# Performance work log

Measured on AMD Instinct MI355X. Metric: run time of the kernel, lower is better.

The kernel has to match this reference:

```python
import jax, jax.numpy as jnp
import numpy as np
from jax import lax

CHUNK = 128
EPS = 1e-6


def rmsnorm(x, w, eps=EPS):
    var = jnp.mean(jnp.square(x.astype(jnp.float32)), axis=-1, keepdims=True)
    return (x * lax.rsqrt(var + eps)).astype(x.dtype) * w


def linear_attn(q, k, v, slopes):
    """Decay-based (lightning/RetNet-style) causal linear attention.
    q,k,v: [B,H,S,D]; slopes: [H,1,1] positive per-head decay rates.
    out[i] = sum_{j<=i} exp(-s*(i-j)) * (q_i . k_j) * v_j, via chunked scan.
    """
    B, H, S, D = q.shape
    C = CHUNK
    nC = S // C
    s = slopes.reshape(1, H, 1, 1).astype(jnp.float32)  # [1,H,1,1]
    t = jnp.arange(C, dtype=jnp.float32)
    q_dec = jnp.exp(-s * t[None, None, :, None])            # [1,H,C,1] decay for inter-chunk query
    k_dec = jnp.exp(-s * (C - t)[None, None, :, None])      # [1,H,C,1] decay applied to keys entering state
    chunk_dec = jnp.exp(-s * C)                              # [1,H,1,1] whole-chunk state decay
    rel = t[:, None] - t[None, :]                            # [C,C]
    intra_dec = jnp.where(rel >= 0, jnp.exp(-s * rel), 0.0)  # [1,H,C,C] causal intra-chunk decay

    # [nC,B,H,C,D]
    qc = q.reshape(B, H, nC, C, D).transpose(2, 0, 1, 3, 4)
    kc = k.reshape(B, H, nC, C, D).transpose(2, 0, 1, 3, 4)
    vc = v.reshape(B, H, nC, C, D).transpose(2, 0, 1, 3, 4)

    def step(kv, inp):
        qi, ki, vi = inp  # each [B,H,C,D]; kv: [B,H,D,D]
        inter = jnp.einsum('bhcd,bhde->bhce', qi * q_dec, kv)
        scores = jnp.einsum('bhcd,bhed->bhce', qi, ki) * intra_dec  # [B,H,C,C]
        intra = jnp.einsum('bhce,bhed->bhcd', scores, vi)
        kv_new = chunk_dec * kv + jnp.einsum('bhcd,bhce->bhde', ki * k_dec, vi)
        return kv_new, inter + intra

    kv0 = jnp.zeros((B, H, D, D), dtype=jnp.float32)
    _, out = lax.scan(step, kv0, (qc, kc, vc))  # out: [nC,B,H,C,D]
    return out.transpose(1, 2, 0, 3, 4).reshape(B, H, S, D)


def setup_inputs() -> dict:
    key = jax.random.key(0)
    ks = jax.random.split(key, 8)
    B, S, E, H, D = 2, 2048, 2048, 16, 128
    init = 0.02
    hidden_states = jax.random.normal(ks[0], (B, S, E), dtype=jnp.float32)
    attention_mask = jnp.ones((B, S), dtype=jnp.float32)
    # standard ALiBi-like per-head slopes in (0,1]
    slope_rate = (2.0 ** (-8.0 * (jnp.arange(H, dtype=jnp.float32) + 1.0) / H)).reshape(H, 1, 1)
    Wq = jax.random.normal(ks[1], (E, H * D), dtype=jnp.float32) * init
    Wk = jax.random.normal(ks[2], (E, H * D), dtype=jnp.float32) * init
    Wv = jax.random.normal(ks[3], (E, H * D), dtype=jnp.float32) * init
    Wg = jax.random.normal(ks[4], (E, H * D), dtype=jnp.float32) * init
    Wo = jax.random.normal(ks[5], (H * D, E), dtype=jnp.float32) * init
    norm_w = jnp.ones((H * D,), dtype=jnp.float32)
    return {"hidden_states": hidden_states, "attention_mask": attention_mask,
            "slope_rate": slope_rate, "Wq": Wq, "Wk": Wk, "Wv": Wv,
            "Wg": Wg, "Wo": Wo, "norm_w": norm_w}


def reference(hidden_states, attention_mask, slope_rate, Wq, Wk, Wv, Wg, Wo, norm_w):
    B, S, E = hidden_states.shape
    H = slope_rate.shape[0]
    D = Wq.shape[1] // H
    q = (hidden_states @ Wq).reshape(B, S, H, D).transpose(0, 2, 1, 3)
    k = (hidden_states @ Wk).reshape(B, S, H, D).transpose(0, 2, 1, 3)
    v = (hidden_states @ Wv).reshape(B, S, H, D).transpose(0, 2, 1, 3)
    v = v * attention_mask[:, None, :, None]
    out = linear_attn(q, k, v, slope_rate)                      # [B,H,S,D]
    out = out.transpose(0, 2, 1, 3).reshape(B, S, H * D)        # b h n d -> b n (h d)
    out = rmsnorm(out, norm_w)
    out = jax.nn.sigmoid(hidden_states @ Wg) * out
    return out @ Wo
```

## Files before the change

### kernel.cpp

```cpp
#include <hip/hip_runtime.h>
#include <cstdint>
#include <cstddef>

typedef unsigned short u16;
typedef unsigned int   u32;

#define SEQ    2048
#define EDIM   2048
#define HEADS  16
#define DHEAD  128
#define CCH    128
#define NCH    16
#define TOKENS 4096

typedef __attribute__((ext_vector_type(8))) short short8;
typedef __attribute__((ext_vector_type(4))) float floatx4;

__device__ __forceinline__ float b2f(u16 b) {
    u32 u = ((u32)b) << 16; float f; __builtin_memcpy(&f, &u, 4); return f;
}
__device__ __forceinline__ u16 f2b(float f) {
    u32 u; __builtin_memcpy(&u, &f, 4);
    u32 r = (u + 0x7fffu + ((u >> 16) & 1u)) >> 16;
    return (u16)r;
}
__device__ __forceinline__ void unpack8(uint4 u, float* f) {
    f[0] = b2f((u16)(u.x & 0xffff)); f[1] = b2f((u16)(u.x >> 16));
    f[2] = b2f((u16)(u.y & 0xffff)); f[3] = b2f((u16)(u.y >> 16));
    f[4] = b2f((u16)(u.z & 0xffff)); f[5] = b2f((u16)(u.z >> 16));
    f[6] = b2f((u16)(u.w & 0xffff)); f[7] = b2f((u16)(u.w >> 16));
}
__device__ __forceinline__ uint4 pack8(const float* f) {
    uint4 u;
    u.x = (u32)f2b(f[0]) | ((u32)f2b(f[1]) << 16);
    u.y = (u32)f2b(f[2]) | ((u32)f2b(f[3]) << 16);
    u.z = (u32)f2b(f[4]) | ((u32)f2b(f[5]) << 16);
    u.w = (u32)f2b(f[6]) | ((u32)f2b(f[7]) << 16);
    return u;
}

__device__ __forceinline__ void gld_lds16(const u16* g, u16* l) {
    __builtin_amdgcn_global_load_lds((const __attribute__((address_space(1))) void*)g,
                                     (__attribute__((address_space(3))) void*)l, 16, 0, 0);
}

__global__ __launch_bounds__(256) void k_f32_to_bf16(const float* __restrict__ in,
                                                     u16* __restrict__ out) {
    int i = blockIdx.x * 256 + threadIdx.x;
    float4 v = ((const float4*)in)[i];
    uint2 o;
    o.x = (u32)f2b(v.x) | ((u32)f2b(v.y) << 16);
    o.y = (u32)f2b(v.z) | ((u32)f2b(v.w) << 16);
    ((uint2*)out)[i] = o;
}

__global__ void k_transW(const float* __restrict__ W0, const float* __restrict__ W1,
                         const float* __restrict__ W2, const float* __restrict__ W3,
                         const float* __restrict__ W4, u16* __restrict__ out) {
    const float* W;
    int z = blockIdx.z;
    switch (z) {
        case 0: W = W0; break; case 1: W = W1; break; case 2: W = W2; break;
        case 3: W = W3; break; default: W = W4; break;
    }
    __shared__ float tile[32][33];
    int n = blockIdx.x * 32 + threadIdx.x;
    int k = blockIdx.y * 32 + threadIdx.y;
    tile[threadIdx.y][threadIdx.x] = W[(size_t)k * EDIM + n];
    __syncthreads();
    int on = blockIdx.x * 32 + threadIdx.y;
    int ok = blockIdx.y * 32 + threadIdx.x;
    out[(size_t)z * EDIM * EDIM + (size_t)on * EDIM + ok] = f2b(tile[threadIdx.x][threadIdx.y]);
}

__global__ __launch_bounds__(256) void k_gemm(const u16* __restrict__ A,
                                              const u16* __restrict__ Bt,
                                              void* __restrict__ C,
                                              int K, int N,
                                              long long zstrB, long long zstrC,
                                              int out_bf16, int mode,
                                              u16* __restrict__ KdT,
                                              u16* __restrict__ VT,
                                              const float* __restrict__ slopes,
                                              const float* __restrict__ mask) {
    __shared__ u16 As[128 * 64];
    __shared__ u16 Bs[128 * 64];
    int z = blockIdx.z;
    const u16* Bz = Bt + (size_t)z * (size_t)zstrB;
    int m0 = blockIdx.y * 128, n0 = blockIdx.x * 128;
    int tid = threadIdx.x;
    int w = tid >> 6, lane = tid & 63;
    int wr = w >> 1, wc = w & 1;
    int lrow = lane & 15, khalf = lane >> 4;

    floatx4 acc[4][4];
#pragma unroll
    for (int i = 0; i < 4; i++)
#pragma unroll
        for (int j = 0; j < 4; j++) acc[i][j] = (floatx4){0.f, 0.f, 0.f, 0.f};

    const u16* aptr[4];
    const u16* bptr[4];
#pragma unroll
    for (int i = 0; i < 4; i++) {
        int c = tid + i * 256;
        int row = c >> 3, slot = c & 7;
        int g = slot ^ (row & 7);
        aptr[i] = A  + (size_t)(m0 + row) * K + g * 8;
        bptr[i] = Bz + (size_t)(n0 + row) * K + g * 8;
    }
    int aoff[2][4], boff[2][4];
#pragma unroll
    for (int kk = 0; kk < 2; kk++)
#pragma unroll
        for (int i = 0; i < 4; i++) {
            int ra = wr * 64 + i * 16 + lrow;
            int rb = wc * 64 + i * 16 + lrow;
            int gg = kk * 4 + khalf;
            aoff[kk][i] = ra * 64 + ((gg ^ (ra & 7)) * 8);
            boff[kk][i] = rb * 64 + ((gg ^ (rb & 7)) * 8);
        }

    for (int k0 = 0; k0 < K; k0 += 64) {
#pragma unroll
        for (int i = 0; i < 4; i++) {
            gld_lds16(aptr[i] + k0, &As[(tid + i * 256) * 8]);
            gld_lds16(bptr[i] + k0, &Bs[(tid + i * 256) * 8]);
        }
        __syncthreads();
#pragma unroll
        for (int kk = 0; kk < 2; kk++) {
            short8 af[4], bfr[4];
#pragma unroll
            for (int i = 0; i < 4; i++) af[i]  = *(const short8*)&As[aoff[kk][i]];
#pragma unroll
            for (int j = 0; j < 4; j++) bfr[j] = *(const short8*)&Bs[boff[kk][j]];
#pragma unroll
            for (int i = 0; i < 4; i++)
#pragma unroll
                for (int j = 0; j < 4; j++)
                    acc[i][j] = __builtin_amdgcn_mfma_f32_16x16x32_bf16(af[i], bfr[j], acc[i][j], 0, 0, 0);
        }
        __syncthreads();
    }

    int writeVT  = (mode == 1 && z == 2);
    int writeKdT = (mode == 1 && z == 1);

    if (!writeVT) {
        size_t cz = (size_t)z * (size_t)zstrC;
#pragma unroll
        for (int i = 0; i < 4; i++)
#pragma unroll
            for (int j = 0; j < 4; j++) {
                int mrow = m0 + wr * 64 + i * 16 + khalf * 4;
                int ncol = n0 + wc * 64 + j * 16 + lrow;
#pragma unroll
                for (int r = 0; r < 4; r++) {
                    float val = acc[i][j][r];
                    if (out_bf16)
                        ((u16*)C)[cz + (size_t)(mrow + r) * N + ncol] = f2b(val);
                    else
                        ((float*)C)[cz + (size_t)(mrow + r) * N + ncol] = val;
                }
            }
    }
    if (writeVT || writeKdT) {
        int b = blockIdx.y >> 4, cc = blockIdx.y & 15, h = blockIdx.x;
        size_t tile = ((size_t)b * 256 + (size_t)h * 16 + (size_t)cc) * 16384;
        float s = slopes[h];
        u16* dst = (writeVT ? VT : KdT) + tile;
#pragma unroll
        for (int i = 0; i < 4; i++)
#pragma unroll
            for (int j = 0; j < 4; j++) {
                int t0 = wr * 64 + i * 16 + khalf * 4;
                int d  = wc * 64 + j * 16 + lrow;
                u16 pk[4];
#pragma unroll
                for (int r = 0; r < 4; r++) {
                    int t = t0 + r;
                    float sc = writeVT ? mask[(size_t)b * SEQ + cc * CCH + t]
                                       : __expf(-s * (float)(CCH - t));
                    pk[r] = f2b(acc[i][j][r] * sc);
                }
                *(uint2*)&dst[(size_t)d * 128 + t0] = *(const uint2*)pk;
            }
    }
}

__global__ __launch_bounds__(256) void k_kvc(const u16* __restrict__ VT,
                                             const u16* __restrict__ KdT,
                                             u16* __restrict__ kvT) {
    int bid = blockIdx.x, tid = threadIdx.x;
    int w = tid >> 6, lane = tid & 63;
    int wr = w >> 1, wc = w & 1;
    int lrow = lane & 15, khalf = lane >> 4;
    const u16* va = VT  + (size_t)bid * 16384;
    const u16* kb = KdT + (size_t)bid * 16384;
    floatx4 acc[4][4];
#pragma unroll
    for (int i = 0; i < 4; i++)
#pragma unroll
        for (int j = 0; j < 4; j++) acc[i][j] = (floatx4){0.f, 0.f, 0.f, 0.f};
#pragma unroll
    for (int kk = 0; kk < 4; kk++) {
        short8 a[4], bf[4];
#pragma unroll
        for (int i = 0; i < 4; i++)
            a[i] = *(const short8*)(va + (size_t)(wr * 64 + i * 16 + lrow) * 128 + kk * 32 + khalf * 8);
#pragma unroll
        for (int j = 0; j < 4; j++)
            bf[j] = *(const short8*)(kb + (size_t)(wc * 64 + j * 16 + lrow) * 128 + kk * 32 + khalf * 8);
#pragma unroll
        for (int i = 0; i < 4; i++)
#pragma unroll
            for (int j = 0; j < 4; j++)
                acc[i][j] = __builtin_amdgcn_mfma_f32_16x16x32_bf16(a[i], bf[j], acc[i][j], 0, 0, 0);
    }
    u16* o = kvT + (size_t)bid * 16384;
#pragma unroll
    for (int i = 0; i < 4; i++)
#pragma unroll
        for (int j = 0; j < 4; j++)
#pragma unroll
            for (int r = 0; r < 4; r++)
                o[(size_t)(wr * 64 + i * 16 + khalf * 4 + r) * 128 + wc * 64 + j * 16 + lrow] =
                    f2b(acc[i][j][r]);
}

__global__ __launch_bounds__(256) void k_scan(u16* __restrict__ kvbuf,
                                              const float* __restrict__ slopes) {
    int gid = blockIdx.x * 256 + threadIdx.x;
    int idx = gid & 16383;
    int bh = gid >> 14;
    int h = bh & 15;
    float cd = __expf(-slopes[h] * (float)CCH);
    u16* p = kvbuf + (size_t)bh * NCH * 16384 + idx;
    float st = 0.f;
    for (int c = 0; c < NCH; c++) {
        float tmp = b2f(p[(size_t)c * 16384]);
        p[(size_t)c * 16384] = f2b(st);
        st = cd * st + tmp;
    }
}

__global__ __launch_bounds__(256) void k_attn_out(const u16* __restrict__ q,
                                                  const u16* __restrict__ k,
                                                  const u16* __restrict__ VT,
                                                  const u16* __restrict__ kvT,
                                                  const float* __restrict__ slopes,
                                                  u16* __restrict__ attn) {
    __shared__ u16 KS[128 * 136];
    int bid = blockIdx.x;
    int c = bid & 15, h = (bid >> 4) & 15, b = bid >> 8;
    float s = slopes[h];
    int tid = threadIdx.x;
    int w = tid >> 6, lane = tid & 63;
    int wr = w >> 1, wc = w & 1;
    int lrow = lane & 15, khalf = lane >> 4;
    size_t tokbase = (size_t)(b * SEQ + c * CCH);

    {
        const u16* kg = k + tokbase * EDIM + h * DHEAD;
#pragma unroll
        for (int i = 0; i < 8; i++) {
            int cidx = tid + i * 256;
            int t = cidx >> 4, part = (cidx & 15) * 8;
            *(uint4*)&KS[t * 136 + part] = *(const uint4*)(kg + (size_t)t * EDIM + part);
        }
    }
    short8 qa[4][4];
    {
        const u16* qgbase = q + tokbase * EDIM + h * DHEAD;
#pragma unroll
        for (int i = 0; i < 4; i++) {
            const u16* qrow = qgbase + (size_t)(wr * 64 + i * 16 + lrow) * EDIM;
#pragma unroll
            for (int kk = 0; kk < 4; kk++)
                qa[i][kk] = *(const short8*)(qrow + kk * 32 + khalf * 8);
        }
    }
    __syncthreads();

    floatx4 acc[4][4];
#pragma unroll
    for (int i = 0; i < 4; i++)
#pragma unroll
        for (int j = 0; j < 4; j++) acc[i][j] = (floatx4){0.f, 0.f, 0.f, 0.f};
#pragma unroll
    for (int kk = 0; kk < 4; kk++) {
        short8 bf[4];
#pragma unroll
        for (int j = 0; j < 4; j++)
            bf[j] = *(const short8*)&KS[(wc * 64 + j * 16 + lrow) * 136 + kk * 32 + khalf * 8];
#pragma unroll
        for (int i = 0; i < 4; i++)
#pragma unroll
            for (int j = 0; j < 4; j++)
                acc[i][j] = __builtin_amdgcn_mfma_f32_16x16x32_bf16(qa[i][kk], bf[j], acc[i][j], 0, 0, 0);
    }
    __syncthreads();

#pragma unroll
    for (int i = 0; i < 4; i++)
#pragma unroll
        for (int j = 0; j < 4; j++) {
            int tbase = wr * 64 + i * 16 + khalf * 4;
            int u = wc * 64 + j * 16 + lrow;
#pragma unroll
            for (int r = 0; r < 4; r++) {
                int t = tbase + r;
                float val = (t >= u) ? acc[i][j][r] * __expf(-s * (float)(t - u)) : 0.f;
                KS[t * 136 + u] = f2b(val);
            }
        }
    __syncthreads();

#pragma unroll
    for (int i = 0; i < 4; i++)
#pragma unroll
        for (int j = 0; j < 4; j++) acc[i][j] = (floatx4){0.f, 0.f, 0.f, 0.f};
    const u16* st = kvT + (size_t)bid * 16384;
#pragma unroll
    for (int kk = 0; kk < 4; kk++) {
        short8 bf[4];
#pragma unroll
        for (int j = 0; j < 4; j++)
            bf[j] = *(const short8*)(st + (size_t)(wc * 64 + j * 16 + lrow) * 128 + kk * 32 + khalf * 8);
#pragma unroll
        for (int i = 0; i < 4; i++)
#pragma unroll
            for (int j = 0; j < 4; j++)
                acc[i][j] = __builtin_amdgcn_mfma_f32_16x16x32_bf16(qa[i][kk], bf[j], acc[i][j], 0, 0, 0);
    }
#pragma unroll
    for (int i = 0; i < 4; i++)
#pragma unroll
        for (int r = 0; r < 4; r++) {
            float qd = __expf(-s * (float)(wr * 64 + i * 16 + khalf * 4 + r));
#pragma unroll
            for (int j = 0; j < 4; j++) acc[i][j][r] *= qd;
        }
    const u16* vt = VT + (size_t)bid * 16384;
#pragma unroll
    for (int kk = 0; kk < 4; kk++) {
        short8 sa[4], bf[4];
#pragma unroll
        for (int i = 0; i < 4; i++)
            sa[i] = *(const short8*)&KS[(wr * 64 + i * 16 + lrow) * 136 + kk * 32 + khalf * 8];
#pragma unroll
        for (int j = 0; j < 4; j++)
            bf[j] = *(const short8*)(vt + (size_t)(wc * 64 + j * 16 + lrow) * 128 + kk * 32 + khalf * 8);
#pragma unroll
        for (int i = 0; i < 4; i++)
#pragma unroll
            for (int j = 0; j < 4; j++)
                acc[i][j] = __builtin_amdgcn_mfma_f32_16x16x32_bf16(sa[i], bf[j], acc[i][j], 0, 0, 0);
    }

    u16* og = attn + tokbase * EDIM + h * DHEAD;
#pragma unroll
    for (int i = 0; i < 4; i++)
#pragma unroll
        for (int j = 0; j < 4; j++)
#pragma unroll
            for (int r = 0; r < 4; r++)
                og[(size_t)(wr * 64 + i * 16 + khalf * 4 + r) * EDIM + wc * 64 + j * 16 + lrow] =
                    f2b(acc[i][j][r]);
}

__global__ __launch_bounds__(256) void k_rms_gate(const u16* __restrict__ attn,
                                                  const u16* __restrict__ gpre,
                                                  const float* __restrict__ nw,
                                                  u16* __restrict__ out) {
    int n = blockIdx.x, tid = threadIdx.x;
    float a[8];
    unpack8(((const uint4*)(attn + (size_t)n * EDIM))[tid], a);
    float ss = 0.f;
#pragma unroll
    for (int j = 0; j < 8; j++) ss += a[j] * a[j];
#pragma unroll
    for (int o = 32; o > 0; o >>= 1) ss += __shfl_down(ss, o, 64);
    __shared__ float red[5];
    int w = tid >> 6, lane = tid & 63;
    if (lane == 0) red[w] = ss;
    __syncthreads();
    if (tid == 0) red[4] = rsqrtf((red[0] + red[1] + red[2] + red[3]) / 2048.f + 1e-6f);
    __syncthreads();
    float rs = red[4];
    float g[8];
    unpack8(((const uint4*)(gpre + (size_t)n * EDIM))[tid], g);
    const float4* np4 = (const float4*)(nw + tid * 8);
    float4 w0 = np4[0], w1 = np4[1];
    float wv[8] = {w0.x, w0.y, w0.z, w0.w, w1.x, w1.y, w1.z, w1.w};
    float o8[8];
#pragma unroll
    for (int j = 0; j < 8; j++) {
        float sg = 1.f / (1.f + __expf(-g[j]));
        o8[j] = sg * (a[j] * rs * wv[j]);
    }
    ((uint4*)(out + (size_t)n * EDIM))[tid] = pack8(o8);
}

extern "C" void kernel_launch(void* const* d_in, const int* in_sizes, int n_in,
                              void* d_out, int out_size, void* d_ws, size_t ws_size,
                              hipStream_t stream) {
    const float* hs     = (const float*)d_in[0];
    const float* mask   = (const float*)d_in[1];
    const float* slopes = (const float*)d_in[2];
    const float* Wq     = (const float*)d_in[3];
    const float* Wk     = (const float*)d_in[4];
    const float* Wv     = (const float*)d_in[5];
    const float* Wg     = (const float*)d_in[6];
    const float* Wo     = (const float*)d_in[7];
    const float* nw     = (const float*)d_in[8];
    float* out = (float*)d_out;

    char* ws = (char*)d_ws;
    u16* hsb   = (u16*)ws;
    u16* Wt    = (u16*)(ws + 16777216LL);
    u16* qkvg  = (u16*)(ws + 58720256LL);
    u16* kvbuf = (u16*)(ws + 125829120LL);
    u16* attn  = (u16*)(ws + 142606336LL);
    u16* qb  = qkvg;
    u16* kb  = qkvg + 8388608LL;
    u16* VT  = qkvg + 16777216LL;
    u16* gb  = qkvg + 25165824LL;
    u16* KdT = attn;

    k_f32_to_bf16<<<8192, 256, 0, stream>>>(hs, hsb);
    k_transW<<<dim3(64, 64, 5), dim3(32, 32, 1), 0, stream>>>(Wq, Wk, Wv, Wg, Wo, Wt);
    k_gemm<<<dim3(16, 32, 4), 256, 0, stream>>>(hsb, Wt, qkvg, EDIM, EDIM,
                                                (long long)EDIM * EDIM,
                                                (long long)TOKENS * EDIM, 1,
                                                1, KdT, VT, slopes, mask);
    k_kvc<<<512, 256, 0, stream>>>(VT, KdT, kvbuf);
    k_scan<<<2048, 256, 0, stream>>>(kvbuf, slopes);
    k_attn_out<<<512, 256, 0, stream>>>(qb, kb, VT, kvbuf, slopes, attn);
    k_rms_gate<<<TOKENS, 256, 0, stream>>>(attn, gb, nw, hsb);
    k_gemm<<<dim3(16, 32, 1), 256, 0, stream>>>(hsb, Wt + 4LL * 4194304LL, out, EDIM, EDIM,
                                                0LL, 0LL, 0,
                                                0, (u16*)nullptr, (u16*)nullptr, slopes, mask);
}
```

Measured before the change: 458.1 us.

## Double-buffer GEMM LDS tiles with async prefetch and manual waitcnt

Replaces the single-buffered 64-wide K tile in the bf16 GEMM with two 32-wide LDS buffers. The loads for the tile two steps ahead are issued before compute, and raw barriers with vmcnt waits keep one load group in flight, so global-to-LDS transfer overlaps MFMA work. The LDS swizzle is adapted to the 32-wide rows, and launch bounds request 4 blocks per CU to raise occupancy. This trades fewer MFMAs per barrier and the fragility of hand-coded waitcnt values for the overlap.

```diff
diff --git a/kernel.cpp b/kernel.cpp
--- a/kernel.cpp
+++ b/kernel.cpp
@@ -43,6 +43,8 @@
     __builtin_amdgcn_global_load_lds((const __attribute__((address_space(1))) void*)g,
                                      (__attribute__((address_space(3))) void*)l, 16, 0, 0);
 }
+#define CFENCE() __asm__ volatile("" ::: "memory")
+#define RAW_BARRIER() do { CFENCE(); __builtin_amdgcn_s_barrier(); CFENCE(); } while (0)
 
 __global__ __launch_bounds__(256) void k_f32_to_bf16(const float* __restrict__ in,
                                                      u16* __restrict__ out) {
@@ -73,18 +75,18 @@
     out[(size_t)z * EDIM * EDIM + (size_t)on * EDIM + ok] = f2b(tile[threadIdx.x][threadIdx.y]);
 }
 
-__global__ __launch_bounds__(256) void k_gemm(const u16* __restrict__ A,
-                                              const u16* __restrict__ Bt,
-                                              void* __restrict__ C,
-                                              int K, int N,
-                                              long long zstrB, long long zstrC,
-                                              int out_bf16, int mode,
-                                              u16* __restrict__ KdT,
-                                              u16* __restrict__ VT,
-                                              const float* __restrict__ slopes,
-                                              const float* __restrict__ mask) {
-    __shared__ u16 As[128 * 64];
-    __shared__ u16 Bs[128 * 64];
+__global__ __launch_bounds__(256, 4) void k_gemm(const u16* __restrict__ A,
+                                                 const u16* __restrict__ Bt,
+                                                 void* __restrict__ C,
+                                                 int K, int N,
+                                                 long long zstrB, long long zstrC,
+                                                 int out_bf16, int mode,
+                                                 u16* __restrict__ KdT,
+                                                 u16* __restrict__ VT,
+                                                 const float* __restrict__ slopes,
+                                                 const float* __restrict__ mask) {
+    __shared__ u16 As[2][128 * 32];
+    __shared__ u16 Bs[2][128 * 32];
     int z = blockIdx.z;
     const u16* Bz = Bt + (size_t)z * (size_t)zstrB;
     int m0 = blockIdx.y * 128, n0 = blockIdx.x * 128;
@@ -99,49 +101,60 @@
 #pragma unroll
         for (int j = 0; j < 4; j++) acc[i][j] = (floatx4){0.f, 0.f, 0.f, 0.f};
 
-    const u16* aptr[4];
-    const u16* bptr[4];
-#pragma unroll
-    for (int i = 0; i < 4; i++) {
+    const u16* aptr[2];
+    const u16* bptr[2];
+    int loff[2];
+#pragma unroll
+    for (int i = 0; i < 2; i++) {
         int c = tid + i * 256;
-        int row = c >> 3, slot = c & 7;
-        int g = slot ^ (row & 7);
+        int row = c >> 2, slot = c & 3;
+        int g = slot ^ ((row >> 1) & 3);
         aptr[i] = A  + (size_t)(m0 + row) * K + g * 8;
         bptr[i] = Bz + (size_t)(n0 + row) * K + g * 8;
-    }
-    int aoff[2][4], boff[2][4];
-#pragma unroll
-    for (int kk = 0; kk < 2; kk++)
-#pragma unroll
-        for (int i = 0; i < 4; i++) {
-            int ra = wr * 64 + i * 16 + lrow;
-            int rb = wc * 64 + i * 16 + lrow;
-            int gg = kk * 4 + khalf;
-            aoff[kk][i] = ra * 64 + ((gg ^ (ra & 7)) * 8);
-            boff[kk][i] = rb * 64 + ((gg ^ (rb & 7)) * 8);
+        loff[i] = c * 8;
+    }
+    int aoff[4], boff[4];
+#pragma unroll
+    for (int i = 0; i < 4; i++) {
+        int ra = wr * 64 + i * 16 + lrow;
+        int rb = wc * 64 + i * 16 + lrow;
+        aoff[i] = ra * 32 + ((khalf ^ ((ra >> 1) & 3)) * 8);
+        boff[i] = rb * 32 + ((khalf ^ ((rb >> 1) & 3)) * 8);
+    }
+
+    int nIter = K >> 5;
+#pragma unroll
+    for (int i = 0; i < 2; i++) gld_lds16(aptr[i] + 0,  &As[0][loff[i]]);
+#pragma unroll
+    for (int i = 0; i < 2; i++) gld_lds16(bptr[i] + 0,  &Bs[0][loff[i]]);
+#pragma unroll
+    for (int i = 0; i < 2; i++) gld_lds16(aptr[i] + 32, &As[1][loff[i]]);
+#pragma unroll
+    for (int i = 0; i < 2; i++) gld_lds16(bptr[i] + 32, &Bs[1][loff[i]]);
+
+    for (int it = 0; it < nIter; ++it) {
+        if (it + 1 < nIter) __builtin_amdgcn_s_waitcnt(0xF74);
+        else                __builtin_amdgcn_s_waitcnt(0xF70);
+        RAW_BARRIER();
+        int buf = it & 1;
+        short8 af[4], bfr[4];
+#pragma unroll
+        for (int i = 0; i < 4; i++) af[i]  = *(const short8*)&As[buf][aoff[i]];
+#pragma unroll
+        for (int j = 0; j < 4; j++) bfr[j] = *(const short8*)&Bs[buf][boff[j]];
+#pragma unroll
+        for (int i = 0; i < 4; i++)
+#pragma unroll
+            for (int j = 0; j < 4; j++)
+                acc[i][j] = __builtin_amdgcn_mfma_f32_16x16x32_bf16(af[i], bfr[j], acc[i][j], 0, 0, 0);
+        RAW_BARRIER();
+        if (it + 2 < nIter) {
+            int k0 = (it + 2) * 32;
+#pragma unroll
+            for (int i = 0; i < 2; i++) gld_lds16(aptr[i] + k0, &As[buf][loff[i]]);
+#pragma unroll
+            for (int i = 0; i < 2; i++) gld_lds16(bptr[i] + k0, &Bs[buf][loff[i]]);
         }
-
-    for (int k0 = 0; k0 < K; k0 += 64) {
-#pragma unroll
-        for (int i = 0; i < 4; i++) {
-            gld_lds16(aptr[i] + k0, &As[(tid + i * 256) * 8]);
-            gld_lds16(bptr[i] + k0, &Bs[(tid + i * 256) * 8]);
-        }
-        __syncthreads();
-#pragma unroll
-        for (int kk = 0; kk < 2; kk++) {
-            short8 af[4], bfr[4];
-#pragma unroll
-            for (int i = 0; i < 4; i++) af[i]  = *(const short8*)&As[aoff[kk][i]];
-#pragma unroll
-            for (int j = 0; j < 4; j++) bfr[j] = *(const short8*)&Bs[boff[kk][j]];
-#pragma unroll
-            for (int i = 0; i < 4; i++)
-#pragma unroll
-                for (int j = 0; j < 4; j++)
-                    acc[i][j] = __builtin_amdgcn_mfma_f32_16x16x32_bf16(af[i], bfr[j], acc[i][j], 0, 0, 0);
-        }
-        __syncthreads();
     }
 
     int writeVT  = (mode == 1 && z == 2);
```

New measurement: 439.2 us. 4.1% less time.
